# Performance work log

Hardware: AMD Instinct MI355X
Metric: run time of the kernel (lower is better)

Reference implementation:

```python
import jax, jax.numpy as jnp
import numpy as np

B, T, D_IN, H = 32768, 10, 81, 128
TM1 = T - 1


def setup_inputs() -> dict:
    key = jax.random.key(0)
    ks = jax.random.split(key, 7)
    s = 1.0 / np.sqrt(H)
    u = lambda k, shape: jax.random.uniform(k, shape, jnp.float32, -s, s)
    return {
        "input_data": jax.random.normal(ks[0], (B, TM1, D_IN), jnp.float32),
        # attn_linear: nn.Linear(2H + T - 1, 1) -> weight stored as vector, scalar bias
        "W_attn": u(ks[1], (2 * H + TM1,)),
        "b_attn": u(ks[2], ()),
        # LSTM params, PyTorch layout: (4H, D_in), (4H, H), gate order i,f,g,o
        "W_ih": u(ks[3], (4 * H, D_IN)),
        "W_hh": u(ks[4], (4 * H, H)),
        "b_ih": u(ks[5], (4 * H,)),
        "b_hh": u(ks[6], (4 * H,)),
    }


def reference(input_data, W_attn, b_attn, W_ih, W_hh, b_ih, b_hh):
    Bc, Tm1, D = input_data.shape
    Hc = W_hh.shape[1]
    # Split attn weight into hidden / cell / driving-series parts.
    # Original: attn_linear(cat([h bcast over D, c bcast over D, input_data.permute(0,2,1)]))
    # Since h,c are identical across the D axis, their contribution is a per-batch scalar.
    Wh, Wc, Wx = W_attn[:Hc], W_attn[Hc:2 * Hc], W_attn[2 * Hc:]
    # Time-invariant part: each driving series' full history dotted with Wx -> (B, D)
    pre = jnp.einsum('btd,t->bd', input_data, Wx) + b_attn

    def step(carry, x_t):
        h, c = carry  # (B, H) each
        logits = pre + (h @ Wh + c @ Wc)[:, None]          # (B, D)
        attn = jax.nn.softmax(logits, axis=1)               # softmax over input features
        w_in = attn * x_t                                   # (B, D) weighted input
        gates = w_in @ W_ih.T + b_ih + h @ W_hh.T + b_hh    # (B, 4H)
        i, f, g, o = jnp.split(gates, 4, axis=1)
        c2 = jax.nn.sigmoid(f) * c + jax.nn.sigmoid(i) * jnp.tanh(g)
        h2 = jax.nn.sigmoid(o) * jnp.tanh(c2)
        return (h2, c2), (w_in, h2)

    h0 = jnp.zeros((Bc, Hc), input_data.dtype)
    (_, _), (wts, enc) = jax.lax.scan(step, (h0, h0), jnp.swapaxes(input_data, 0, 1))
    input_weighted = jnp.swapaxes(wts, 0, 1)  # (B, T-1, D)
    input_encoded = jnp.swapaxes(enc, 0, 1)   # (B, T-1, H)
    return input_weighted, input_encoded
```

## Files before the change

### kernel.cpp

```cpp
#include <hip/hip_runtime.h>
#include <hip/hip_bf16.h>


namespace {

constexpr int kB    = 32768;
constexpr int kT    = 9;
constexpr int kD    = 81;
constexpr int kH    = 128;
constexpr int kG    = 512;
constexpr int kK    = 209;
constexpr int kKPad = 224;
constexpr int kNB   = 32;
constexpr int kTh   = 256;
constexpr int kAS   = 232;

constexpr int kWsWtBytes  = kG * kKPad * 2;
constexpr int kWsBiasOff  = kWsWtBytes;
constexpr int kWsWxOff    = kWsBiasOff + kG * 4;
constexpr int kWsBAttnOff = kWsWxOff + 16 * 4;

typedef __bf16 bf16x8 __attribute__((ext_vector_type(8)));
typedef float  f32x4  __attribute__((ext_vector_type(4)));

__device__ __forceinline__ float sigf(float x) {
  return __builtin_amdgcn_rcpf(1.f + __expf(-x));
}
__device__ __forceinline__ float tanhfast(float x) {
  return 1.f - 2.f * __builtin_amdgcn_rcpf(1.f + __expf(2.f * x));
}

__global__ void prep_kernel(const float* __restrict__ W_attn,
                            const float* __restrict__ b_attn,
                            const float* __restrict__ W_ih,
                            const float* __restrict__ W_hh,
                            const float* __restrict__ b_ih,
                            const float* __restrict__ b_hh,
                            unsigned char* __restrict__ ws) {
  __bf16* Wt   = reinterpret_cast<__bf16*>(ws);
  float* biasp = reinterpret_cast<float*>(ws + kWsBiasOff);
  float* wxp   = reinterpret_cast<float*>(ws + kWsWxOff);
  float* bap   = reinterpret_cast<float*>(ws + kWsBAttnOff);
  int tid = blockIdx.x * blockDim.x + threadIdx.x;
  int nth = gridDim.x * blockDim.x;
  for (int idx = tid; idx < kG * kKPad; idx += nth) {
    int p = idx / kKPad, k = idx - p * kKPad;
    int u = p >> 2, q = p & 3, g = q * kH + u;
    float v = 0.f;
    if (k < kD)      v = W_ih[g * kD + k];
    else if (k < kK) v = W_hh[g * kH + (k - kD)];
    Wt[idx] = (__bf16)v;
  }
  if (tid < kG) {
    int u = tid >> 2, q = tid & 3, g = q * kH + u;
    biasp[tid] = b_ih[g] + b_hh[g];
  }
  if (tid >= kG && tid < kG + 16) {
    int t = tid - kG;
    wxp[t] = (t < kT) ? W_attn[2 * kH + t] : 0.f;
  }
  if (tid == kG + 16) bap[0] = b_attn[0];
}

__global__ __launch_bounds__(kTh, 2) void enc_main(
    const float* __restrict__ x,
    const unsigned char* __restrict__ ws,
    float* __restrict__ out_w,
    float* __restrict__ out_h) {
  __shared__ __align__(16) __bf16 ash[kNB][kAS];
  __shared__ __align__(16) __bf16 asl[kNB][kAS];
  __shared__ __align__(16) float bias_s[kG];
  __shared__ float red[kNB][8];
  __shared__ float wx_s[16];
  __shared__ float battn_s;

  const int tid = threadIdx.x;
  const int b0  = blockIdx.x * kNB;
  const __bf16* Wt = reinterpret_cast<const __bf16*>(ws);

  if (tid < 16) wx_s[tid] = reinterpret_cast<const float*>(ws + kWsWxOff)[tid];
  if (tid == 16) battn_s = reinterpret_cast<const float*>(ws + kWsBAttnOff)[0];
  bias_s[tid]       = reinterpret_cast<const float*>(ws + kWsBiasOff)[tid];
  bias_s[tid + 256] = reinterpret_cast<const float*>(ws + kWsBiasOff)[tid + 256];
  for (int i = tid; i < kNB * kAS; i += kTh) {
    (&ash[0][0])[i] = (__bf16)0.f;
    (&asl[0][0])[i] = (__bf16)0.f;
  }
  __syncthreads();

  const int sb = tid >> 3;
  const int sq = tid & 7;
  float attn[11];
  {
    float lmax = -3.4e38f;
    const size_t xbase = (size_t)(b0 + sb) * kT * kD;
#pragma unroll
    for (int m = 0; m < 11; ++m) {
      int d = sq + 8 * m;
      float s = -3.4e38f;
      if (d < kD) {
        s = battn_s;
#pragma unroll
        for (int t = 0; t < kT; ++t)
          s += x[xbase + t * kD + d] * wx_s[t];
        lmax = fmaxf(lmax, s);
      }
      attn[m] = s;
    }
    red[sb][sq] = lmax;
    __syncthreads();
    float gmax = red[sb][0];
#pragma unroll
    for (int r = 1; r < 8; ++r) gmax = fmaxf(gmax, red[sb][r]);
    __syncthreads();
    float lsum = 0.f;
#pragma unroll
    for (int m = 0; m < 11; ++m) {
      float e = __expf(attn[m] - gmax);
      attn[m] = e;
      lsum += e;
    }
    red[sb][sq] = lsum;
    __syncthreads();
    float tot = 0.f;
#pragma unroll
    for (int r = 0; r < 8; ++r) tot += red[sb][r];
    float inv = 1.0f / tot;
#pragma unroll
    for (int m = 0; m < 11; ++m) attn[m] *= inv;
  }

  const int lane = tid & 63;
  const int wv   = tid >> 6;
  const int lb   = lane & 15;
  const int kg   = lane >> 4;
  const __bf16* wrow = Wt + (size_t)(wv * 128 + lb) * kKPad;

  float c_reg[2][8];
#pragma unroll
  for (int bt = 0; bt < 2; ++bt)
#pragma unroll
    for (int p = 0; p < 8; ++p) c_reg[bt][p] = 0.f;

  for (int t = 0; t < kT; ++t) {
    {
      const size_t xoff = ((size_t)(b0 + sb) * kT + t) * kD;
#pragma unroll
      for (int m = 0; m < 11; ++m) {
        int d = sq + 8 * m;
        if (d < kD) {
          float w = attn[m] * x[xoff + d];
          out_w[xoff + d] = w;
          __bf16 hi = (__bf16)w;
          ash[sb][d] = hi;
          asl[sb][d] = (__bf16)(w - (float)hi);
        }
      }
    }
    __syncthreads();

    f32x4 acc[2][8];
#pragma unroll
    for (int p = 0; p < 8; ++p) {
      f32x4 bv = *reinterpret_cast<const f32x4*>(
          &bias_s[wv * 128 + p * 16 + kg * 4]);
      acc[0][p] = bv;
      acc[1][p] = bv;
    }
#pragma unroll
    for (int ks = 0; ks < kKPad / 32; ++ks) {
      const int k0 = ks * 32 + kg * 8;
      bf16x8 bh0 = *reinterpret_cast<const bf16x8*>(&ash[lb][k0]);
      bf16x8 bl0 = *reinterpret_cast<const bf16x8*>(&asl[lb][k0]);
      bf16x8 bh1 = *reinterpret_cast<const bf16x8*>(&ash[16 + lb][k0]);
      bf16x8 bl1 = *reinterpret_cast<const bf16x8*>(&asl[16 + lb][k0]);
#pragma unroll
      for (int p = 0; p < 8; ++p) {
        bf16x8 wf = *reinterpret_cast<const bf16x8*>(
            wrow + p * (16 * kKPad) + k0);
        acc[0][p] = __builtin_amdgcn_mfma_f32_16x16x32_bf16(wf, bh0, acc[0][p], 0, 0, 0);
        acc[0][p] = __builtin_amdgcn_mfma_f32_16x16x32_bf16(wf, bl0, acc[0][p], 0, 0, 0);
        acc[1][p] = __builtin_amdgcn_mfma_f32_16x16x32_bf16(wf, bh1, acc[1][p], 0, 0, 0);
        acc[1][p] = __builtin_amdgcn_mfma_f32_16x16x32_bf16(wf, bl1, acc[1][p], 0, 0, 0);
      }
    }
    __syncthreads();

#pragma unroll
    for (int bt = 0; bt < 2; ++bt) {
#pragma unroll
      for (int p = 0; p < 8; ++p) {
        f32x4 g4 = acc[bt][p];
        float cn = sigf(g4[1]) * c_reg[bt][p] + sigf(g4[0]) * tanhfast(g4[2]);
        float hn = sigf(g4[3]) * tanhfast(cn);
        c_reg[bt][p] = cn;
        const int b = bt * 16 + lb;
        const int u = wv * 32 + p * 4 + kg;
        out_h[((size_t)(b0 + b) * kT + t) * kH + u] = hn;
        __bf16 hi = (__bf16)hn;
        ash[b][kD + u] = hi;
        asl[b][kD + u] = (__bf16)(hn - (float)hi);
      }
    }
  }
}

}

extern "C" void kernel_launch(void* const* d_in, const int* in_sizes, int n_in,
                              void* d_out, int out_size, void* d_ws, size_t ws_size,
                              hipStream_t stream) {
  (void)in_sizes; (void)n_in; (void)out_size; (void)ws_size;
  const float* x      = (const float*)d_in[0];
  const float* W_attn = (const float*)d_in[1];
  const float* b_attn = (const float*)d_in[2];
  const float* W_ih   = (const float*)d_in[3];
  const float* W_hh   = (const float*)d_in[4];
  const float* b_ih   = (const float*)d_in[5];
  const float* b_hh   = (const float*)d_in[6];
  float* out_w = (float*)d_out;
  float* out_h = out_w + (size_t)kB * kT * kD;
  unsigned char* ws = (unsigned char*)d_ws;

  hipLaunchKernelGGL(prep_kernel, dim3(64), dim3(256), 0, stream,
                     W_attn, b_attn, W_ih, W_hh, b_ih, b_hh, ws);
  hipLaunchKernelGGL(enc_main, dim3(kB / kNB), dim3(kTh), 0, stream,
                     x, ws, out_w, out_h);
}
```

Measured before the change: 648.7 us.

## Double batch tile per block, retile MFMA loop, prefetch x and use nontemporal I/O

Each block now handles 64 batch rows with 512 threads. Each wave covers 64 gate rows across four 16-row batch tiles, so every weight fragment loaded from global memory feeds four batch tiles instead of two, which lowers weight traffic per batch element. The next timestep's x values are prefetched into registers during the current step, and the accumulator is zero-initialised with the bias added in the epilogue. x loads and output stores become nontemporal. The trade-off is more LDS per block and changed occupancy under launch_bounds(512,4).

```diff
diff --git a/kernel.cpp b/kernel.cpp
--- a/kernel.cpp
+++ b/kernel.cpp
@@ -11,8 +11,8 @@
 constexpr int kG    = 512;
 constexpr int kK    = 209;
 constexpr int kKPad = 224;
-constexpr int kNB   = 32;
-constexpr int kTh   = 256;
+constexpr int kNB   = 64;
+constexpr int kTh   = 512;
 constexpr int kAS   = 232;
 
 constexpr int kWsWtBytes  = kG * kKPad * 2;
@@ -62,7 +62,7 @@
   if (tid == kG + 16) bap[0] = b_attn[0];
 }
 
-__global__ __launch_bounds__(kTh, 2) void enc_main(
+__global__ __launch_bounds__(kTh, 4) void enc_main(
     const float* __restrict__ x,
     const unsigned char* __restrict__ ws,
     float* __restrict__ out_w,
@@ -80,8 +80,7 @@
 
   if (tid < 16) wx_s[tid] = reinterpret_cast<const float*>(ws + kWsWxOff)[tid];
   if (tid == 16) battn_s = reinterpret_cast<const float*>(ws + kWsBAttnOff)[0];
-  bias_s[tid]       = reinterpret_cast<const float*>(ws + kWsBiasOff)[tid];
-  bias_s[tid + 256] = reinterpret_cast<const float*>(ws + kWsBiasOff)[tid + 256];
+  bias_s[tid] = reinterpret_cast<const float*>(ws + kWsBiasOff)[tid];
   for (int i = tid; i < kNB * kAS; i += kTh) {
     (&ash[0][0])[i] = (__bf16)0.f;
     (&asl[0][0])[i] = (__bf16)0.f;
@@ -90,10 +89,10 @@
 
   const int sb = tid >> 3;
   const int sq = tid & 7;
+  const size_t xbase = (size_t)(b0 + sb) * kT * kD;
   float attn[11];
   {
     float lmax = -3.4e38f;
-    const size_t xbase = (size_t)(b0 + sb) * kT * kD;
 #pragma unroll
     for (int m = 0; m < 11; ++m) {
       int d = sq + 8 * m;
@@ -102,7 +101,7 @@
         s = battn_s;
 #pragma unroll
         for (int t = 0; t < kT; ++t)
-          s += x[xbase + t * kD + d] * wx_s[t];
+          s += __builtin_nontemporal_load(x + xbase + t * kD + d) * wx_s[t];
         lmax = fmaxf(lmax, s);
       }
       attn[m] = s;
@@ -134,69 +133,86 @@
   const int wv   = tid >> 6;
   const int lb   = lane & 15;
   const int kg   = lane >> 4;
-  const __bf16* wrow = Wt + (size_t)(wv * 128 + lb) * kKPad;
-
-  float c_reg[2][8];
-#pragma unroll
-  for (int bt = 0; bt < 2; ++bt)
-#pragma unroll
-    for (int p = 0; p < 8; ++p) c_reg[bt][p] = 0.f;
+  const __bf16* wrow = Wt + (size_t)(wv * 64 + lb) * kKPad;
+
+  float c_reg[4][4];
+#pragma unroll
+  for (int bt = 0; bt < 4; ++bt)
+#pragma unroll
+    for (int p = 0; p < 4; ++p) c_reg[bt][p] = 0.f;
+
+  float xr[11];
+#pragma unroll
+  for (int m = 0; m < 11; ++m) {
+    int d = sq + 8 * m;
+    xr[m] = (d < kD) ? __builtin_nontemporal_load(x + xbase + d) : 0.f;
+  }
 
   for (int t = 0; t < kT; ++t) {
     {
-      const size_t xoff = ((size_t)(b0 + sb) * kT + t) * kD;
+      const size_t xoff = xbase + (size_t)t * kD;
 #pragma unroll
       for (int m = 0; m < 11; ++m) {
         int d = sq + 8 * m;
         if (d < kD) {
-          float w = attn[m] * x[xoff + d];
-          out_w[xoff + d] = w;
+          float w = attn[m] * xr[m];
+          __builtin_nontemporal_store(w, out_w + xoff + d);
           __bf16 hi = (__bf16)w;
           ash[sb][d] = hi;
           asl[sb][d] = (__bf16)(w - (float)hi);
         }
       }
-    }
-    __syncthreads();
-
-    f32x4 acc[2][8];
-#pragma unroll
-    for (int p = 0; p < 8; ++p) {
-      f32x4 bv = *reinterpret_cast<const f32x4*>(
-          &bias_s[wv * 128 + p * 16 + kg * 4]);
-      acc[0][p] = bv;
-      acc[1][p] = bv;
-    }
+      if (t + 1 < kT) {
+#pragma unroll
+        for (int m = 0; m < 11; ++m) {
+          int d = sq + 8 * m;
+          if (d < kD)
+            xr[m] = __builtin_nontemporal_load(x + xoff + kD + d);
+        }
+      }
+    }
+    __syncthreads();
+
+    f32x4 acc[4][4];
+#pragma unroll
+    for (int bt = 0; bt < 4; ++bt)
+#pragma unroll
+      for (int p = 0; p < 4; ++p) acc[bt][p] = (f32x4){0.f, 0.f, 0.f, 0.f};
+
 #pragma unroll
     for (int ks = 0; ks < kKPad / 32; ++ks) {
       const int k0 = ks * 32 + kg * 8;
-      bf16x8 bh0 = *reinterpret_cast<const bf16x8*>(&ash[lb][k0]);
-      bf16x8 bl0 = *reinterpret_cast<const bf16x8*>(&asl[lb][k0]);
-      bf16x8 bh1 = *reinterpret_cast<const bf16x8*>(&ash[16 + lb][k0]);
-      bf16x8 bl1 = *reinterpret_cast<const bf16x8*>(&asl[16 + lb][k0]);
-#pragma unroll
-      for (int p = 0; p < 8; ++p) {
-        bf16x8 wf = *reinterpret_cast<const bf16x8*>(
-            wrow + p * (16 * kKPad) + k0);
-        acc[0][p] = __builtin_amdgcn_mfma_f32_16x16x32_bf16(wf, bh0, acc[0][p], 0, 0, 0);
-        acc[0][p] = __builtin_amdgcn_mfma_f32_16x16x32_bf16(wf, bl0, acc[0][p], 0, 0, 0);
-        acc[1][p] = __builtin_amdgcn_mfma_f32_16x16x32_bf16(wf, bh1, acc[1][p], 0, 0, 0);
-        acc[1][p] = __builtin_amdgcn_mfma_f32_16x16x32_bf16(wf, bl1, acc[1][p], 0, 0, 0);
-      }
-    }
-    __syncthreads();
-
-#pragma unroll
-    for (int bt = 0; bt < 2; ++bt) {
-#pragma unroll
-      for (int p = 0; p < 8; ++p) {
+      bf16x8 wf[4];
+#pragma unroll
+      for (int p = 0; p < 4; ++p)
+        wf[p] = *reinterpret_cast<const bf16x8*>(wrow + p * (16 * kKPad) + k0);
+#pragma unroll
+      for (int bt = 0; bt < 4; ++bt) {
+        bf16x8 bh = *reinterpret_cast<const bf16x8*>(&ash[bt * 16 + lb][k0]);
+        bf16x8 bl = *reinterpret_cast<const bf16x8*>(&asl[bt * 16 + lb][k0]);
+#pragma unroll
+        for (int p = 0; p < 4; ++p) {
+          acc[bt][p] = __builtin_amdgcn_mfma_f32_16x16x32_bf16(wf[p], bh, acc[bt][p], 0, 0, 0);
+          acc[bt][p] = __builtin_amdgcn_mfma_f32_16x16x32_bf16(wf[p], bl, acc[bt][p], 0, 0, 0);
+        }
+      }
+    }
+    __syncthreads();
+
+#pragma unroll
+    for (int p = 0; p < 4; ++p) {
+      const int u = wv * 16 + p * 4 + kg;
+      f32x4 bv = *reinterpret_cast<const f32x4*>(&bias_s[wv * 64 + p * 16 + kg * 4]);
+#pragma unroll
+      for (int bt = 0; bt < 4; ++bt) {
         f32x4 g4 = acc[bt][p];
-        float cn = sigf(g4[1]) * c_reg[bt][p] + sigf(g4[0]) * tanhfast(g4[2]);
-        float hn = sigf(g4[3]) * tanhfast(cn);
+        float cn = sigf(g4[1] + bv[1]) * c_reg[bt][p] +
+                   sigf(g4[0] + bv[0]) * tanhfast(g4[2] + bv[2]);
+        float hn = sigf(g4[3] + bv[3]) * tanhfast(cn);
         c_reg[bt][p] = cn;
         const int b = bt * 16 + lb;
-        const int u = wv * 32 + p * 4 + kg;
-        out_h[((size_t)(b0 + b) * kT + t) * kH + u] = hn;
+        __builtin_nontemporal_store(
+            hn, out_h + ((size_t)(b0 + b) * kT + t) * kH + u);
         __bf16 hi = (__bf16)hn;
         ash[b][kD + u] = hi;
         asl[b][kD + u] = (__bf16)(hn - (float)hi);
```

New measurement: 1.176 ms. 1.81x slower.

## Coalesce h output via LDS, prefetch x, reorder K layout, nontemporal stores

Applied to the files above, without the earlier changes.

Reorders the packed weight K dimension so h occupies columns 0-127 and the weighted input follows at 128, letting h be written to LDS aligned. Output h is now reconstructed from the hi/lo bf16 pair in LDS and written as coalesced 16-byte nontemporal stores instead of scattered scalar stores. Input x for the next step is prefetched into registers during the current step, and the weight fragments are loaded once per k-slice and reused across both batch tiles. The cost is an extra barrier per step and reconstructing h from split bf16, which may differ slightly from the fp32 value.

```diff
diff --git a/kernel.cpp b/kernel.cpp
--- a/kernel.cpp
+++ b/kernel.cpp
@@ -9,7 +9,6 @@
 constexpr int kD    = 81;
 constexpr int kH    = 128;
 constexpr int kG    = 512;
-constexpr int kK    = 209;
 constexpr int kKPad = 224;
 constexpr int kNB   = 32;
 constexpr int kTh   = 256;
@@ -47,8 +46,8 @@
     int p = idx / kKPad, k = idx - p * kKPad;
     int u = p >> 2, q = p & 3, g = q * kH + u;
     float v = 0.f;
-    if (k < kD)      v = W_ih[g * kD + k];
-    else if (k < kK) v = W_hh[g * kH + (k - kD)];
+    if (k < kH)               v = W_hh[g * kH + k];
+    else if (k < kH + kD)     v = W_ih[g * kD + (k - kH)];
     Wt[idx] = (__bf16)v;
   }
   if (tid < kG) {
@@ -90,10 +89,10 @@
 
   const int sb = tid >> 3;
   const int sq = tid & 7;
+  const size_t xbase = (size_t)(b0 + sb) * kT * kD;
   float attn[11];
   {
     float lmax = -3.4e38f;
-    const size_t xbase = (size_t)(b0 + sb) * kT * kD;
 #pragma unroll
     for (int m = 0; m < 11; ++m) {
       int d = sq + 8 * m;
@@ -142,18 +141,32 @@
 #pragma unroll
     for (int p = 0; p < 8; ++p) c_reg[bt][p] = 0.f;
 
+  float xr[11];
+#pragma unroll
+  for (int m = 0; m < 11; ++m) {
+    int d = sq + 8 * m;
+    xr[m] = (d < kD) ? x[xbase + d] : 0.f;
+  }
+
   for (int t = 0; t < kT; ++t) {
     {
-      const size_t xoff = ((size_t)(b0 + sb) * kT + t) * kD;
+      const size_t xoff = xbase + (size_t)t * kD;
 #pragma unroll
       for (int m = 0; m < 11; ++m) {
         int d = sq + 8 * m;
         if (d < kD) {
-          float w = attn[m] * x[xoff + d];
-          out_w[xoff + d] = w;
+          float w = attn[m] * xr[m];
+          __builtin_nontemporal_store(w, out_w + xoff + d);
           __bf16 hi = (__bf16)w;
-          ash[sb][d] = hi;
-          asl[sb][d] = (__bf16)(w - (float)hi);
+          ash[sb][kH + d] = hi;
+          asl[sb][kH + d] = (__bf16)(w - (float)hi);
+        }
+      }
+      if (t + 1 < kT) {
+#pragma unroll
+        for (int m = 0; m < 11; ++m) {
+          int d = sq + 8 * m;
+          if (d < kD) xr[m] = x[xoff + kD + d];
         }
       }
     }
@@ -170,37 +183,61 @@
 #pragma unroll
     for (int ks = 0; ks < kKPad / 32; ++ks) {
       const int k0 = ks * 32 + kg * 8;
-      bf16x8 bh0 = *reinterpret_cast<const bf16x8*>(&ash[lb][k0]);
-      bf16x8 bl0 = *reinterpret_cast<const bf16x8*>(&asl[lb][k0]);
-      bf16x8 bh1 = *reinterpret_cast<const bf16x8*>(&ash[16 + lb][k0]);
-      bf16x8 bl1 = *reinterpret_cast<const bf16x8*>(&asl[16 + lb][k0]);
-#pragma unroll
-      for (int p = 0; p < 8; ++p) {
-        bf16x8 wf = *reinterpret_cast<const bf16x8*>(
-            wrow + p * (16 * kKPad) + k0);
-        acc[0][p] = __builtin_amdgcn_mfma_f32_16x16x32_bf16(wf, bh0, acc[0][p], 0, 0, 0);
-        acc[0][p] = __builtin_amdgcn_mfma_f32_16x16x32_bf16(wf, bl0, acc[0][p], 0, 0, 0);
-        acc[1][p] = __builtin_amdgcn_mfma_f32_16x16x32_bf16(wf, bh1, acc[1][p], 0, 0, 0);
-        acc[1][p] = __builtin_amdgcn_mfma_f32_16x16x32_bf16(wf, bl1, acc[1][p], 0, 0, 0);
-      }
-    }
-    __syncthreads();
-
-#pragma unroll
-    for (int bt = 0; bt < 2; ++bt) {
-#pragma unroll
-      for (int p = 0; p < 8; ++p) {
+      bf16x8 wf[8];
+#pragma unroll
+      for (int p = 0; p < 8; ++p)
+        wf[p] = *reinterpret_cast<const bf16x8*>(wrow + p * (16 * kKPad) + k0);
+#pragma unroll
+      for (int bt = 0; bt < 2; ++bt) {
+        bf16x8 bh = *reinterpret_cast<const bf16x8*>(&ash[bt * 16 + lb][k0]);
+        bf16x8 bl = *reinterpret_cast<const bf16x8*>(&asl[bt * 16 + lb][k0]);
+#pragma unroll
+        for (int p = 0; p < 8; ++p) {
+          acc[bt][p] = __builtin_amdgcn_mfma_f32_16x16x32_bf16(wf[p], bh, acc[bt][p], 0, 0, 0);
+          acc[bt][p] = __builtin_amdgcn_mfma_f32_16x16x32_bf16(wf[p], bl, acc[bt][p], 0, 0, 0);
+        }
+      }
+    }
+    __syncthreads();
+
+#pragma unroll
+    for (int p = 0; p < 8; ++p) {
+      const int u = wv * 32 + p * 4 + kg;
+#pragma unroll
+      for (int bt = 0; bt < 2; ++bt) {
         f32x4 g4 = acc[bt][p];
         float cn = sigf(g4[1]) * c_reg[bt][p] + sigf(g4[0]) * tanhfast(g4[2]);
         float hn = sigf(g4[3]) * tanhfast(cn);
         c_reg[bt][p] = cn;
         const int b = bt * 16 + lb;
-        const int u = wv * 32 + p * 4 + kg;
-        out_h[((size_t)(b0 + b) * kT + t) * kH + u] = hn;
         __bf16 hi = (__bf16)hn;
-        ash[b][kD + u] = hi;
-        asl[b][kD + u] = (__bf16)(hn - (float)hi);
-      }
+        ash[b][u] = hi;
+        asl[b][u] = (__bf16)(hn - (float)hi);
+      }
+    }
+    __syncthreads();
+
+    {
+      const int hb = tid >> 3;
+      const int u0 = (tid & 7) * 16;
+      float* orow = out_h + ((size_t)(b0 + hb) * kT + t) * kH + u0;
+      bf16x8 h0 = *reinterpret_cast<const bf16x8*>(&ash[hb][u0]);
+      bf16x8 h1 = *reinterpret_cast<const bf16x8*>(&ash[hb][u0 + 8]);
+      bf16x8 l0 = *reinterpret_cast<const bf16x8*>(&asl[hb][u0]);
+      bf16x8 l1 = *reinterpret_cast<const bf16x8*>(&asl[hb][u0 + 8]);
+      f32x4 v;
+#pragma unroll
+      for (int i = 0; i < 4; ++i) v[i] = (float)h0[i] + (float)l0[i];
+      __builtin_nontemporal_store(v, reinterpret_cast<f32x4*>(orow));
+#pragma unroll
+      for (int i = 0; i < 4; ++i) v[i] = (float)h0[4 + i] + (float)l0[4 + i];
+      __builtin_nontemporal_store(v, reinterpret_cast<f32x4*>(orow + 4));
+#pragma unroll
+      for (int i = 0; i < 4; ++i) v[i] = (float)h1[i] + (float)l1[i];
+      __builtin_nontemporal_store(v, reinterpret_cast<f32x4*>(orow + 8));
+#pragma unroll
+      for (int i = 0; i < 4; ++i) v[i] = (float)h1[4 + i] + (float)l1[4 + i];
+      __builtin_nontemporal_store(v, reinterpret_cast<f32x4*>(orow + 12));
     }
   }
 }
```

After: 1.005 ms. +54.9%, slower.
